# Optimization experiments

Hardware: AMD Instinct MI355X
Metric: run time of the kernel (lower is better)

The kernel has to match this reference:

```python
import math
from itertools import combinations_with_replacement
import jax, jax.numpy as jnp
import numpy as np

# ---- static config (matches init_kwargs) ----
SPECIES_LIST = [1, 6, 8]
S = len(SPECIES_LIST)
N_MAX = 8
L_MAX = 4
CUTOFF = 5.0
B, N = 4, 512

SPECIES = jnp.asarray(SPECIES_LIST, dtype=jnp.int64 if jax.config.jax_enable_x64 else jnp.int32)
PAIR_IDS = np.array(list(combinations_with_replacement(range(S), 2)), dtype=np.int32)  # (P,2)
P = PAIR_IDS.shape[0]

# orthonormalization matrix W (deterministic buffer)
def _ortho_W(n_max):
    a = np.arange(1, n_max + 1, dtype=np.float64)
    Smat = np.sqrt((5 + 2 * a[:, None]) * (5 + 2 * a[None, :])) / (5 + a[:, None] + a[None, :])
    w, v = np.linalg.eigh(Smat)
    return (v @ np.diag(w ** -0.5) @ v.T).astype(np.float32)
W_ORTHO = jnp.asarray(_ortho_W(N_MAX))

# per-l power-spectrum prefactor pi*sqrt(8/(2l+1))
PS_NORM = jnp.asarray([math.pi * math.sqrt(8.0 / (2 * l + 1)) for l in range(L_MAX + 1)], dtype=jnp.float32)
# selector: which of the 25 flattened (l,m) components belong to degree l
_l_of_m = np.concatenate([np.full(2 * l + 1, l) for l in range(L_MAX + 1)])
L_SEL = jnp.asarray((_l_of_m[None, :] == np.arange(L_MAX + 1)[:, None]).astype(np.float32))  # (L,25)
# sqrt(2) on strict-upper (n,p) entries (applied before triu gather)
_offd = np.ones((N_MAX, N_MAX), dtype=np.float32)
_offd[np.triu_indices(N_MAX, 1)] = math.sqrt(2.0)
OFFD = jnp.asarray(_offd)
IU_R, IU_C = np.triu_indices(N_MAX)
PAIR_F = jnp.asarray(np.where(PAIR_IDS[:, 0] != PAIR_IDS[:, 1], math.sqrt(2.0), 1.0).astype(np.float32))


def real_sph_harm(u):
    """Real spherical harmonics (integral normalization, homogeneous polynomial form)
    for l=0..4, evaluated on u (..., 3). Returns (..., 25). Zero vector -> l>0 vanish."""
    x, y, z = u[..., 0], u[..., 1], u[..., 2]
    x2, y2, z2 = x * x, y * y, z * z
    r2 = x2 + y2 + z2
    pi = math.pi
    s = math.sqrt
    Y = [
        jnp.full_like(x, 0.5 * s(1 / pi)),
        s(3 / (4 * pi)) * y, s(3 / (4 * pi)) * z, s(3 / (4 * pi)) * x,
        0.5 * s(15 / pi) * x * y,
        0.5 * s(15 / pi) * y * z,
        0.25 * s(5 / pi) * (3 * z2 - r2),
        0.5 * s(15 / pi) * x * z,
        0.25 * s(15 / pi) * (x2 - y2),
        0.25 * s(35 / (2 * pi)) * y * (3 * x2 - y2),
        0.5 * s(105 / pi) * x * y * z,
        0.25 * s(21 / (2 * pi)) * y * (5 * z2 - r2),
        0.25 * s(7 / pi) * z * (5 * z2 - 3 * r2),
        0.25 * s(21 / (2 * pi)) * x * (5 * z2 - r2),
        0.25 * s(105 / pi) * z * (x2 - y2),
        0.25 * s(35 / (2 * pi)) * x * (x2 - 3 * y2),
        0.75 * s(35 / pi) * x * y * (x2 - y2),
        0.75 * s(35 / (2 * pi)) * y * z * (3 * x2 - y2),
        0.75 * s(5 / pi) * x * y * (7 * z2 - r2),
        0.75 * s(5 / (2 * pi)) * y * z * (7 * z2 - 3 * r2),
        (3.0 / 16.0) * s(1 / pi) * (35 * z2 * z2 - 30 * z2 * r2 + 3 * r2 * r2),
        0.75 * s(5 / (2 * pi)) * x * z * (7 * z2 - 3 * r2),
        (3.0 / 8.0) * s(5 / pi) * (x2 - y2) * (7 * z2 - r2),
        0.75 * s(35 / (2 * pi)) * x * z * (x2 - 3 * y2),
        (3.0 / 16.0) * s(35 / pi) * (x2 * x2 - 6 * x2 * y2 + y2 * y2),
    ]
    return jnp.stack(Y, axis=-1)


def soap_forward(pos, Z):
    b, n, _ = pos.shape
    # pairwise within each frame: dvec[b,i,j] = pos[b,i] - pos[b,j]  (dst - src)
    dvec = pos[:, :, None, :] - pos[:, None, :, :]          # (B,N,N,3)
    d2 = jnp.sum(dvec * dvec, axis=-1)
    dist = jnp.where(d2 > 0, jnp.sqrt(jnp.where(d2 > 0, d2, 1.0)), 0.0)
    u = dvec / jnp.where(dist > 0, dist, 1.0)[..., None]
    Y = real_sph_harm(u) * (4.0 * math.pi)                  # (B,N,N,25)
    # radial basis (l-independent in this module); cutoff mask folds in dist>=cutoff pairs
    alpha = jnp.arange(1, N_MAX + 1, dtype=pos.dtype)
    norm_factor = jnp.sqrt(CUTOFF ** (2 * alpha + 5) / (2 * alpha + 5))
    dr = jnp.maximum(CUTOFF - dist, 0.0)[..., None]
    basis = dr ** (alpha + 2) / norm_factor * (dist < CUTOFF).astype(pos.dtype)[..., None]
    g = basis @ W_ORTHO.T                                   # (B,N,N,n_max)
    # per-species scatter-add over source atoms j -> density coefficients c
    s_oh = (Z[..., None] == SPECIES).astype(pos.dtype)      # (B,N,S)
    c = jnp.einsum('bjs,bijn,bijm->bisnm', s_oh, g, Y)      # (B,N,S,n_max,25)
    # power spectrum: sum over m within each l
    ps = jnp.einsum('bisnm,bitpm,lm->bistlnp', c, c, L_SEL) # (B,N,S,S,L,n,n)
    ps = ps[:, :, PAIR_IDS[:, 0], PAIR_IDS[:, 1]]           # (B,N,P,L,n,n)
    ps = ps * PAIR_F[:, None, None, None] * PS_NORM[:, None, None] * OFFD
    desc = ps[..., IU_R, IU_C]                              # (B,N,P,L,36)
    return desc.reshape(b, n, -1)                           # (B,N,1080)


def setup_inputs() -> dict:
    key = jax.random.key(0)
    k1, k2 = jax.random.split(key)
    pos = jax.random.uniform(k1, (B, N, 3), dtype=jnp.float32) * 22.0
    Z = SPECIES[jax.random.randint(k2, (B, N), 0, S)]
    return {'pos': pos, 'Z': Z}


def reference(pos, Z):
    return soap_forward(pos, Z)
```

## Files before the change

### kernel.cpp

```cpp
#include <hip/hip_runtime.h>
#include <cmath>

#define NMAX   8
#define NM     25
#define ROWW   40
#define NOUT   1080
#define C2SZ   1440

struct Params {
    float W[NMAX * NMAX];
    float invnorm[NMAX];
    float ycoef[NM];
    float lscale[5];
    float pairf[6];
};

__device__ __forceinline__ void neighbor_compute(const Params& prm,
                                                 float dx, float dy, float dz,
                                                 float* __restrict__ row) {
    const float d2 = dx * dx + dy * dy + dz * dz;
    const float dist = sqrtf(d2);
    const float inv  = dist > 0.f ? 1.f / dist : 0.f;
    const float x = dx * inv, y = dy * inv, z = dz * inv;
    const float x2 = x * x, y2 = y * y, z2 = z * z;
    const float r2 = x2 + y2 + z2;

    const float dr = 5.f - dist;
    float bas[NMAX];
    float drp = dr * dr * dr;
#pragma unroll
    for (int a = 0; a < NMAX; ++a) { bas[a] = drp * prm.invnorm[a]; drp *= dr; }
    float g[NMAX];
#pragma unroll
    for (int n = 0; n < NMAX; ++n) {
        float acc = 0.f;
#pragma unroll
        for (int a = 0; a < NMAX; ++a) acc += bas[a] * prm.W[n * NMAX + a];
        g[n] = acc;
    }

    float Yv[NM];
    Yv[0]  = prm.ycoef[0];
    Yv[1]  = prm.ycoef[1]  * y;
    Yv[2]  = prm.ycoef[2]  * z;
    Yv[3]  = prm.ycoef[3]  * x;
    Yv[4]  = prm.ycoef[4]  * x * y;
    Yv[5]  = prm.ycoef[5]  * y * z;
    Yv[6]  = prm.ycoef[6]  * (3.f * z2 - r2);
    Yv[7]  = prm.ycoef[7]  * x * z;
    Yv[8]  = prm.ycoef[8]  * (x2 - y2);
    Yv[9]  = prm.ycoef[9]  * y * (3.f * x2 - y2);
    Yv[10] = prm.ycoef[10] * x * y * z;
    Yv[11] = prm.ycoef[11] * y * (5.f * z2 - r2);
    Yv[12] = prm.ycoef[12] * z * (5.f * z2 - 3.f * r2);
    Yv[13] = prm.ycoef[13] * x * (5.f * z2 - r2);
    Yv[14] = prm.ycoef[14] * z * (x2 - y2);
    Yv[15] = prm.ycoef[15] * x * (x2 - 3.f * y2);
    Yv[16] = prm.ycoef[16] * x * y * (x2 - y2);
    Yv[17] = prm.ycoef[17] * y * z * (3.f * x2 - y2);
    Yv[18] = prm.ycoef[18] * x * y * (7.f * z2 - r2);
    Yv[19] = prm.ycoef[19] * y * z * (7.f * z2 - 3.f * r2);
    Yv[20] = prm.ycoef[20] * (35.f * z2 * z2 - 30.f * z2 * r2 + 3.f * r2 * r2);
    Yv[21] = prm.ycoef[21] * x * z * (7.f * z2 - 3.f * r2);
    Yv[22] = prm.ycoef[22] * (x2 - y2) * (7.f * z2 - r2);
    Yv[23] = prm.ycoef[23] * x * z * (x2 - 3.f * y2);
    Yv[24] = prm.ycoef[24] * (x2 * x2 - 6.f * x2 * y2 + y2 * y2);

    float4* q = (float4*)row;
    q[0] = make_float4(g[0], g[1], g[2], g[3]);
    q[1] = make_float4(g[4], g[5], g[6], g[7]);
    q[2] = make_float4(Yv[0], Yv[8],  Yv[16], Yv[24]);
    q[3] = make_float4(Yv[1], Yv[9],  Yv[17], 0.f);
    q[4] = make_float4(Yv[2], Yv[10], Yv[18], 0.f);
    q[5] = make_float4(Yv[3], Yv[11], Yv[19], 0.f);
    q[6] = make_float4(Yv[4], Yv[12], Yv[20], 0.f);
    q[7] = make_float4(Yv[5], Yv[13], Yv[21], 0.f);
    q[8] = make_float4(Yv[6], Yv[14], Yv[22], 0.f);
    q[9] = make_float4(Yv[7], Yv[15], Yv[23], 0.f);
}

__global__ __launch_bounds__(64)
void soap_kernel(const float* __restrict__ pos, const int* __restrict__ Z,
                 float* __restrict__ out, Params prm) {
    __shared__ __align__(16) float gys[64 * ROWW];
    __shared__ float4 dA[64];
    __shared__ float4 dB[64];
    __shared__ __align__(16) float c2[C2SZ];
    __shared__ int spl[64];

    const int lane = threadIdx.x;
    const int site = blockIdx.x;
    const int jbase = (site >> 9) << 9;

    const float xi = pos[site * 3 + 0];
    const float yi = pos[site * 3 + 1];
    const float zi = pos[site * 3 + 2];

    {
        float4* c4 = (float4*)c2;
        const float4 zz4 = make_float4(0.f, 0.f, 0.f, 0.f);
#pragma unroll
        for (int i = 0; i < 5; ++i) c4[i * 64 + lane] = zz4;
        if (lane < 40) c4[320 + lane] = zz4;
    }

    const unsigned long long ltm = (1ull << lane) - 1ull;
    int mtot = 0;
#pragma unroll
    for (int it = 0; it < 8; ++it) {
        const int ja = jbase + it * 64 + lane;
        const float dx = xi - pos[ja * 3 + 0];
        const float dy = yi - pos[ja * 3 + 1];
        const float dz = zi - pos[ja * 3 + 2];
        const float d2 = dx * dx + dy * dy + dz * dz;
        const bool pr = d2 < 25.0f;
        const unsigned long long mk = __ballot(pr);
        if (pr) {
            const int sl = mtot + __popcll(mk & ltm);
            if (sl < 64) dA[sl] = make_float4(dx, dy, dz, (float)ja);
        }
        mtot += __popcll(mk);
    }
    const int M = mtot;

    const int n_own = lane & 7;
    const int mrow  = lane >> 3;
    float a0[4] = {0.f,0.f,0.f,0.f};
    float a1[4] = {0.f,0.f,0.f,0.f};
    float a2[4] = {0.f,0.f,0.f,0.f};

    if (M <= 64) {
        float4 v = make_float4(0.f, 0.f, 0.f, 0.f);
        int sp = -1;
        if (lane < M) {
            v = dA[lane];
            const int zz = Z[(int)v.w];
            sp = (zz == 1) ? 0 : (zz == 6) ? 1 : 2;
        }
        const unsigned long long b0 = __ballot(sp == 0);
        const unsigned long long b1 = __ballot(sp == 1);
        const unsigned long long b2 = __ballot(sp == 2);
        const int R1 = __popcll(b0);
        const int R2 = R1 + __popcll(b1);
        int np = -1;
        if (sp == 0)      np = __popcll(b0 & ltm);
        else if (sp == 1) np = R1 + __popcll(b1 & ltm);
        else if (sp == 2) np = R2 + __popcll(b2 & ltm);
        if (np >= 0) dB[np] = v;

        if (lane < M) {
            const float4 u = dB[lane];
            neighbor_compute(prm, u.x, u.y, u.z, &gys[lane * ROWW]);
        }

        const float* yb = &gys[8 + 4 * mrow];
#pragma unroll 2
        for (int sl = 0; sl < R1; ++sl) {
            const float g = gys[sl * ROWW + n_own];
            const float4 y4 = *(const float4*)&yb[sl * ROWW];
            a0[0] += g * y4.x; a0[1] += g * y4.y; a0[2] += g * y4.z; a0[3] += g * y4.w;
        }
#pragma unroll 2
        for (int sl = R1; sl < R2; ++sl) {
            const float g = gys[sl * ROWW + n_own];
            const float4 y4 = *(const float4*)&yb[sl * ROWW];
            a1[0] += g * y4.x; a1[1] += g * y4.y; a1[2] += g * y4.z; a1[3] += g * y4.w;
        }
#pragma unroll 2
        for (int sl = R2; sl < M; ++sl) {
            const float g = gys[sl * ROWW + n_own];
            const float4 y4 = *(const float4*)&yb[sl * ROWW];
            a2[0] += g * y4.x; a2[1] += g * y4.y; a2[2] += g * y4.z; a2[3] += g * y4.w;
        }
    } else {
        for (int it = 0; it < 8; ++it) {
            const int ja = jbase + it * 64 + lane;
            const float dx = xi - pos[ja * 3 + 0];
            const float dy = yi - pos[ja * 3 + 1];
            const float dz = zi - pos[ja * 3 + 2];
            const float d2 = dx * dx + dy * dy + dz * dz;
            const bool pr = d2 < 25.0f;
            const unsigned long long mk = __ballot(pr);
            const int cnt = __popcll(mk);
            if (pr) {
                const int sl = __popcll(mk & ltm);
                dA[sl] = make_float4(dx, dy, dz, 0.f);
                const int zz = Z[ja];
                spl[sl] = (zz == 1) ? 0 : (zz == 6) ? 1 : 2;
            }
            if (lane < cnt) {
                const float4 u = dA[lane];
                neighbor_compute(prm, u.x, u.y, u.z, &gys[lane * ROWW]);
            }
            const float* yb = &gys[8 + 4 * mrow];
            for (int sl = 0; sl < cnt; ++sl) {
                const int ss = spl[sl];
                const float g = gys[sl * ROWW + n_own];
                const float4 y4 = *(const float4*)&yb[sl * ROWW];
                if (ss == 0) {
                    a0[0] += g * y4.x; a0[1] += g * y4.y; a0[2] += g * y4.z; a0[3] += g * y4.w;
                } else if (ss == 1) {
                    a1[0] += g * y4.x; a1[1] += g * y4.y; a1[2] += g * y4.z; a1[3] += g * y4.w;
                } else {
                    a2[0] += g * y4.x; a2[1] += g * y4.y; a2[2] += g * y4.z; a2[3] += g * y4.w;
                }
            }
        }
    }

#pragma unroll
    for (int k = 0; k < 4; ++k) {
        const int m = mrow + 8 * k;
        if (m < NM) {
            const int l  = (int)sqrtf((float)m);
            const int kk = m - l * l;
            const int idx = l * 288 + n_own * 12 + kk;
            c2[idx      ] = a0[k];
            c2[idx +  96] = a1[k];
            c2[idx + 192] = a2[k];
        }
    }

#pragma unroll
    for (int it = 0; it < 17; ++it) {
        const int o = it * 64 + lane;
        if (o < NOUT) {
            const int q   = o / 180;
            const int rem = o - q * 180;
            const int l   = rem / 36;
            const int t   = rem - l * 36;
            const int n = (int)((17.0f - sqrtf((float)(289 - 8 * t))) * 0.5f);
            const int p = t - ((n * (17 - n)) >> 1) + n;
            const int s1 = (q < 3) ? 0 : ((q < 5) ? 1 : 2);
            const int s2 = (q < 3) ? q : ((q < 5) ? (q - 2) : 2);
            const float4* ra = (const float4*)&c2[l * 288 + s1 * 96 + n * 12];
            const float4* rb = (const float4*)&c2[l * 288 + s2 * 96 + p * 12];
            const float4 A0 = ra[0], B0 = rb[0];
            const float4 A1 = ra[1], B1 = rb[1];
            const float4 A2 = ra[2], B2 = rb[2];
            float sum = A0.x * B0.x + A0.y * B0.y + A0.z * B0.z + A0.w * B0.w
                      + A1.x * B1.x + A1.y * B1.y + A1.z * B1.z + A1.w * B1.w
                      + A2.x * B2.x + A2.y * B2.y + A2.z * B2.z + A2.w * B2.w;
            float sc = prm.pairf[q] * prm.lscale[l];
            if (n != p) sc *= 1.41421356237309515f;
            out[site * NOUT + o] = sum * sc;
        }
    }
}

extern "C" void kernel_launch(void* const* d_in, const int* in_sizes, int n_in,
                              void* d_out, int out_size, void* d_ws, size_t ws_size,
                              hipStream_t stream) {
    const float* pos = (const float*)d_in[0];
    const int*   Z   = (const int*)d_in[1];
    float*       out = (float*)d_out;
    const int nsite  = in_sizes[1];

    Params prm;

    double A[8][8], V[8][8];
    for (int i = 0; i < 8; ++i)
        for (int j = 0; j < 8; ++j) {
            const double ai = i + 1.0, aj = j + 1.0;
            A[i][j] = sqrt((5.0 + 2.0 * ai) * (5.0 + 2.0 * aj)) / (5.0 + ai + aj);
            V[i][j] = (i == j) ? 1.0 : 0.0;
        }
    for (int sweep = 0; sweep < 30; ++sweep) {
        for (int p = 0; p < 8; ++p)
            for (int q = p + 1; q < 8; ++q) {
                const double apq = A[p][q];
                if (fabs(apq) < 1e-300) continue;
                const double phi = 0.5 * atan2(2.0 * apq, A[q][q] - A[p][p]);
                const double c = cos(phi), s = sin(phi);
                for (int k = 0; k < 8; ++k) {
                    const double akp = A[k][p], akq = A[k][q];
                    A[k][p] = c * akp - s * akq;
                    A[k][q] = s * akp + c * akq;
                }
                for (int k = 0; k < 8; ++k) {
                    const double apk = A[p][k], aqk = A[q][k];
                    A[p][k] = c * apk - s * aqk;
                    A[q][k] = s * apk + c * aqk;
                }
                for (int k = 0; k < 8; ++k) {
                    const double vkp = V[k][p], vkq = V[k][q];
                    V[k][p] = c * vkp - s * vkq;
                    V[k][q] = s * vkp + c * vkq;
                }
            }
    }
    for (int i = 0; i < 8; ++i)
        for (int j = 0; j < 8; ++j) {
            double acc = 0.0;
            for (int k = 0; k < 8; ++k) acc += V[i][k] * V[j][k] / sqrt(A[k][k]);
            prm.W[i * 8 + j] = (float)acc;
        }

    for (int a = 0; a < 8; ++a)
        prm.invnorm[a] = (float)(1.0 / sqrt(pow(5.0, 2.0 * a + 7.0) / (2.0 * a + 7.0)));

    const double pi = 3.14159265358979323846;
    const double fp = 4.0 * pi;
    double yc[NM];
    yc[0]  = 0.5 * sqrt(1.0 / pi);
    yc[1]  = yc[2] = yc[3] = sqrt(3.0 / (4.0 * pi));
    yc[4]  = yc[5] = yc[7] = 0.5 * sqrt(15.0 / pi);
    yc[6]  = 0.25 * sqrt(5.0 / pi);
    yc[8]  = 0.25 * sqrt(15.0 / pi);
    yc[9]  = yc[15] = 0.25 * sqrt(35.0 / (2.0 * pi));
    yc[10] = 0.5 * sqrt(105.0 / pi);
    yc[11] = yc[13] = 0.25 * sqrt(21.0 / (2.0 * pi));
    yc[12] = 0.25 * sqrt(7.0 / pi);
    yc[14] = 0.25 * sqrt(105.0 / pi);
    yc[16] = 0.75 * sqrt(35.0 / pi);
    yc[17] = yc[23] = 0.75 * sqrt(35.0 / (2.0 * pi));
    yc[18] = 0.75 * sqrt(5.0 / pi);
    yc[19] = yc[21] = 0.75 * sqrt(5.0 / (2.0 * pi));
    yc[20] = 3.0 / 16.0 * sqrt(1.0 / pi);
    yc[22] = 3.0 / 8.0 * sqrt(5.0 / pi);
    yc[24] = 3.0 / 16.0 * sqrt(35.0 / pi);
    for (int m = 0; m < NM; ++m) prm.ycoef[m] = (float)(yc[m] * fp);

    for (int l = 0; l <= 4; ++l) prm.lscale[l] = (float)(pi * sqrt(8.0 / (2.0 * l + 1.0)));
    const float rt2 = 1.41421356237309515f;
    prm.pairf[0] = 1.f; prm.pairf[1] = rt2; prm.pairf[2] = rt2;
    prm.pairf[3] = 1.f; prm.pairf[4] = rt2; prm.pairf[5] = 1.f;

    soap_kernel<<<nsite, 64, 0, stream>>>(pos, Z, out, prm);
}
```

Baseline: 16.84 us.

## Split density accumulation across per-species wavefronts in 256-thread blocks

Each block now runs four wavefronts. Three of them each filter neighbours for one species and accumulate that species' density coefficients, in a smaller chunked shared buffer. A block-wide sync follows, then all four waves compute the power-spectrum items using a compacted per-l layout that skips the zero padding. The aim is to parallelise the serial per-site accumulation and cut wasted FMAs on padded m entries. In exchange, every wave recomputes the distance filter, the fourth wave sits idle during accumulation, and the larger blocks may lower occupancy.

```diff
diff --git a/kernel.cpp b/kernel.cpp
--- a/kernel.cpp
+++ b/kernel.cpp
@@ -1,11 +1,13 @@
 #include <hip/hip_runtime.h>
 #include <cmath>
 
-#define NMAX   8
-#define NM     25
-#define ROWW   40
-#define NOUT   1080
-#define C2SZ   1440
+#define NMAX    8
+#define NM      25
+#define GSLOTS  24
+#define ROWW    44
+#define NOUT    1080
+#define CROW    36
+#define CSLICE  288
 
 struct Params {
     float W[NMAX * NMAX];
@@ -79,171 +81,133 @@
     q[9] = make_float4(Yv[7], Yv[15], Yv[23], 0.f);
 }
 
-__global__ __launch_bounds__(64)
+__global__ __launch_bounds__(256)
 void soap_kernel(const float* __restrict__ pos, const int* __restrict__ Z,
                  float* __restrict__ out, Params prm) {
-    __shared__ __align__(16) float gys[64 * ROWW];
-    __shared__ float4 dA[64];
-    __shared__ float4 dB[64];
-    __shared__ __align__(16) float c2[C2SZ];
-    __shared__ int spl[64];
-
-    const int lane = threadIdx.x;
+    __shared__ float4 dA[3][64];
+    __shared__ __align__(16) float gys[3][GSLOTS * ROWW];
+    __shared__ __align__(16) float c2[3 * CSLICE];
+
+    const int tid  = threadIdx.x;
+    const int lane = tid & 63;
+    const int w    = tid >> 6;
     const int site = blockIdx.x;
     const int jbase = (site >> 9) << 9;
+    const unsigned long long ltm = (1ull << lane) - 1ull;
 
     const float xi = pos[site * 3 + 0];
     const float yi = pos[site * 3 + 1];
     const float zi = pos[site * 3 + 2];
 
-    {
-        float4* c4 = (float4*)c2;
-        const float4 zz4 = make_float4(0.f, 0.f, 0.f, 0.f);
-#pragma unroll
-        for (int i = 0; i < 5; ++i) c4[i * 64 + lane] = zz4;
-        if (lane < 40) c4[320 + lane] = zz4;
-    }
-
-    const unsigned long long ltm = (1ull << lane) - 1ull;
-    int mtot = 0;
-#pragma unroll
-    for (int it = 0; it < 8; ++it) {
-        const int ja = jbase + it * 64 + lane;
-        const float dx = xi - pos[ja * 3 + 0];
-        const float dy = yi - pos[ja * 3 + 1];
-        const float dz = zi - pos[ja * 3 + 2];
-        const float d2 = dx * dx + dy * dy + dz * dz;
-        const bool pr = d2 < 25.0f;
-        const unsigned long long mk = __ballot(pr);
-        if (pr) {
-            const int sl = mtot + __popcll(mk & ltm);
-            if (sl < 64) dA[sl] = make_float4(dx, dy, dz, (float)ja);
-        }
-        mtot += __popcll(mk);
-    }
-    const int M = mtot;
-
-    const int n_own = lane & 7;
-    const int mrow  = lane >> 3;
-    float a0[4] = {0.f,0.f,0.f,0.f};
-    float a1[4] = {0.f,0.f,0.f,0.f};
-    float a2[4] = {0.f,0.f,0.f,0.f};
-
-    if (M <= 64) {
-        float4 v = make_float4(0.f, 0.f, 0.f, 0.f);
-        int sp = -1;
-        if (lane < M) {
-            v = dA[lane];
-            const int zz = Z[(int)v.w];
-            sp = (zz == 1) ? 0 : (zz == 6) ? 1 : 2;
-        }
-        const unsigned long long b0 = __ballot(sp == 0);
-        const unsigned long long b1 = __ballot(sp == 1);
-        const unsigned long long b2 = __ballot(sp == 2);
-        const int R1 = __popcll(b0);
-        const int R2 = R1 + __popcll(b1);
-        int np = -1;
-        if (sp == 0)      np = __popcll(b0 & ltm);
-        else if (sp == 1) np = R1 + __popcll(b1 & ltm);
-        else if (sp == 2) np = R2 + __popcll(b2 & ltm);
-        if (np >= 0) dB[np] = v;
-
-        if (lane < M) {
-            const float4 u = dB[lane];
-            neighbor_compute(prm, u.x, u.y, u.z, &gys[lane * ROWW]);
-        }
-
-        const float* yb = &gys[8 + 4 * mrow];
-#pragma unroll 2
-        for (int sl = 0; sl < R1; ++sl) {
-            const float g = gys[sl * ROWW + n_own];
-            const float4 y4 = *(const float4*)&yb[sl * ROWW];
-            a0[0] += g * y4.x; a0[1] += g * y4.y; a0[2] += g * y4.z; a0[3] += g * y4.w;
-        }
-#pragma unroll 2
-        for (int sl = R1; sl < R2; ++sl) {
-            const float g = gys[sl * ROWW + n_own];
-            const float4 y4 = *(const float4*)&yb[sl * ROWW];
-            a1[0] += g * y4.x; a1[1] += g * y4.y; a1[2] += g * y4.z; a1[3] += g * y4.w;
-        }
-#pragma unroll 2
-        for (int sl = R2; sl < M; ++sl) {
-            const float g = gys[sl * ROWW + n_own];
-            const float4 y4 = *(const float4*)&yb[sl * ROWW];
-            a2[0] += g * y4.x; a2[1] += g * y4.y; a2[2] += g * y4.z; a2[3] += g * y4.w;
-        }
-    } else {
+    if (w < 3) {
+        const int s = w;
+        float4* cz = (float4*)&c2[s * CSLICE];
+        cz[lane & 63] = make_float4(0.f, 0.f, 0.f, 0.f);
+        if (lane < 8) cz[64 + lane] = make_float4(0.f, 0.f, 0.f, 0.f);
+
+        int mtot = 0;
+#pragma unroll
         for (int it = 0; it < 8; ++it) {
             const int ja = jbase + it * 64 + lane;
             const float dx = xi - pos[ja * 3 + 0];
             const float dy = yi - pos[ja * 3 + 1];
             const float dz = zi - pos[ja * 3 + 2];
             const float d2 = dx * dx + dy * dy + dz * dz;
-            const bool pr = d2 < 25.0f;
+            const int zz = Z[ja];
+            const int sp = (zz == 1) ? 0 : (zz == 6) ? 1 : 2;
+            const bool pr = (d2 < 25.0f) && (sp == s);
             const unsigned long long mk = __ballot(pr);
-            const int cnt = __popcll(mk);
             if (pr) {
-                const int sl = __popcll(mk & ltm);
-                dA[sl] = make_float4(dx, dy, dz, 0.f);
+                const int sl = mtot + __popcll(mk & ltm);
+                if (sl < 64) dA[s][sl] = make_float4(dx, dy, dz, 0.f);
+            }
+            mtot += __popcll(mk);
+        }
+        const int Ms = mtot;
+
+        const int n_own = lane & 7;
+        const int mrow  = lane >> 3;
+        float a[4] = {0.f, 0.f, 0.f, 0.f};
+        const float* yb = &gys[s][8 + 4 * mrow];
+
+        if (Ms <= 64) {
+            for (int rb = 0; rb < Ms; rb += GSLOTS) {
+                const int cnt = min(GSLOTS, Ms - rb);
+                if (lane < cnt) {
+                    const float4 u = dA[s][rb + lane];
+                    neighbor_compute(prm, u.x, u.y, u.z, &gys[s][lane * ROWW]);
+                }
+                for (int sl = 0; sl < cnt; ++sl) {
+                    const float g  = gys[s][sl * ROWW + n_own];
+                    const float4 y4 = *(const float4*)&yb[sl * ROWW];
+                    a[0] += g * y4.x; a[1] += g * y4.y; a[2] += g * y4.z; a[3] += g * y4.w;
+                }
+            }
+        } else {
+            for (int it = 0; it < 8; ++it) {
+                const int ja = jbase + it * 64 + lane;
+                const float dx = xi - pos[ja * 3 + 0];
+                const float dy = yi - pos[ja * 3 + 1];
+                const float dz = zi - pos[ja * 3 + 2];
+                const float d2 = dx * dx + dy * dy + dz * dz;
                 const int zz = Z[ja];
-                spl[sl] = (zz == 1) ? 0 : (zz == 6) ? 1 : 2;
-            }
-            if (lane < cnt) {
-                const float4 u = dA[lane];
-                neighbor_compute(prm, u.x, u.y, u.z, &gys[lane * ROWW]);
-            }
-            const float* yb = &gys[8 + 4 * mrow];
-            for (int sl = 0; sl < cnt; ++sl) {
-                const int ss = spl[sl];
-                const float g = gys[sl * ROWW + n_own];
-                const float4 y4 = *(const float4*)&yb[sl * ROWW];
-                if (ss == 0) {
-                    a0[0] += g * y4.x; a0[1] += g * y4.y; a0[2] += g * y4.z; a0[3] += g * y4.w;
-                } else if (ss == 1) {
-                    a1[0] += g * y4.x; a1[1] += g * y4.y; a1[2] += g * y4.z; a1[3] += g * y4.w;
-                } else {
-                    a2[0] += g * y4.x; a2[1] += g * y4.y; a2[2] += g * y4.z; a2[3] += g * y4.w;
-                }
-            }
-        }
-    }
-
-#pragma unroll
-    for (int k = 0; k < 4; ++k) {
-        const int m = mrow + 8 * k;
-        if (m < NM) {
-            const int l  = (int)sqrtf((float)m);
-            const int kk = m - l * l;
-            const int idx = l * 288 + n_own * 12 + kk;
-            c2[idx      ] = a0[k];
-            c2[idx +  96] = a1[k];
-            c2[idx + 192] = a2[k];
-        }
-    }
-
-#pragma unroll
-    for (int it = 0; it < 17; ++it) {
-        const int o = it * 64 + lane;
-        if (o < NOUT) {
-            const int q   = o / 180;
-            const int rem = o - q * 180;
-            const int l   = rem / 36;
-            const int t   = rem - l * 36;
-            const int n = (int)((17.0f - sqrtf((float)(289 - 8 * t))) * 0.5f);
-            const int p = t - ((n * (17 - n)) >> 1) + n;
+                const int sp = (zz == 1) ? 0 : (zz == 6) ? 1 : 2;
+                const bool pr = (d2 < 25.0f) && (sp == s);
+                const unsigned long long mk = __ballot(pr);
+                const int cnt0 = __popcll(mk);
+                if (pr) dA[s][__popcll(mk & ltm)] = make_float4(dx, dy, dz, 0.f);
+                for (int rb = 0; rb < cnt0; rb += GSLOTS) {
+                    const int cnt = min(GSLOTS, cnt0 - rb);
+                    if (lane < cnt) {
+                        const float4 u = dA[s][rb + lane];
+                        neighbor_compute(prm, u.x, u.y, u.z, &gys[s][lane * ROWW]);
+                    }
+                    for (int sl = 0; sl < cnt; ++sl) {
+                        const float g  = gys[s][sl * ROWW + n_own];
+                        const float4 y4 = *(const float4*)&yb[sl * ROWW];
+                        a[0] += g * y4.x; a[1] += g * y4.y; a[2] += g * y4.z; a[3] += g * y4.w;
+                    }
+                }
+            }
+        }
+
+#pragma unroll
+        for (int k = 0; k < 4; ++k) {
+            const int m = mrow + 8 * k;
+            if (m < NM) {
+                const int l  = (int)sqrtf((float)m);
+                const int kk = m - l * l;
+                const int lofs = (l < 2) ? 4 * l : 8 * (l - 1);
+                c2[s * CSLICE + n_own * CROW + lofs + kk] = a[k];
+            }
+        }
+    }
+
+    __syncthreads();
+
+    if (lane < 36) {
+        const int t = lane;
+        const int n = (int)((17.0f - sqrtf((float)(289 - 8 * t))) * 0.5f);
+        const int p = t - ((n * (17 - n)) >> 1) + n;
+        const float npf = (n != p) ? 1.41421356237309515f : 1.0f;
+        const int start = (w < 2) ? 8 * w : 16 + 7 * (w - 2);
+        const int icnt  = (w < 2) ? 8 : 7;
+        for (int ii = 0; ii < icnt; ++ii) {
+            const int item = start + ii;
+            const int q = (item * 13) >> 6;
+            const int l = item - 5 * q;
             const int s1 = (q < 3) ? 0 : ((q < 5) ? 1 : 2);
             const int s2 = (q < 3) ? q : ((q < 5) ? (q - 2) : 2);
-            const float4* ra = (const float4*)&c2[l * 288 + s1 * 96 + n * 12];
-            const float4* rb = (const float4*)&c2[l * 288 + s2 * 96 + p * 12];
-            const float4 A0 = ra[0], B0 = rb[0];
-            const float4 A1 = ra[1], B1 = rb[1];
-            const float4 A2 = ra[2], B2 = rb[2];
-            float sum = A0.x * B0.x + A0.y * B0.y + A0.z * B0.z + A0.w * B0.w
-                      + A1.x * B1.x + A1.y * B1.y + A1.z * B1.z + A1.w * B1.w
-                      + A2.x * B2.x + A2.y * B2.y + A2.z * B2.z + A2.w * B2.w;
-            float sc = prm.pairf[q] * prm.lscale[l];
-            if (n != p) sc *= 1.41421356237309515f;
-            out[site * NOUT + o] = sum * sc;
+            const int lofs = (l < 2) ? 4 * l : 8 * (l - 1);
+            const int nq   = (l < 2) ? 1 : ((l < 4) ? 2 : 3);
+            const float4* ra = (const float4*)&c2[s1 * CSLICE + n * CROW + lofs];
+            const float4* rb = (const float4*)&c2[s2 * CSLICE + p * CROW + lofs];
+            float sum = 0.f;
+            for (int j = 0; j < nq; ++j) {
+                const float4 av = ra[j], bv = rb[j];
+                sum += av.x * bv.x + av.y * bv.y + av.z * bv.z + av.w * bv.w;
+            }
+            out[site * NOUT + q * 180 + l * 36 + t] = sum * prm.pairf[q] * prm.lscale[l] * npf;
         }
     }
 }
@@ -326,5 +290,5 @@
     prm.pairf[0] = 1.f; prm.pairf[1] = rt2; prm.pairf[2] = rt2;
     prm.pairf[3] = 1.f; prm.pairf[4] = rt2; prm.pairf[5] = 1.f;
 
-    soap_kernel<<<nsite, 64, 0, stream>>>(pos, Z, out, prm);
+    soap_kernel<<<nsite, 256, 0, stream>>>(pos, Z, out, prm);
 }
```

Result: slower. 21.29 us (+26.4%).

## Pad species groups to four rows, unroll accumulation, compact c2 layout

Applied to the files above, without the earlier changes.

The species index is now computed during the neighbour scan and packed into the float4, so the second gather of Z is no longer needed. Each species group is padded to a multiple of four zero-filled rows, which lets the accumulation loop process four neighbours per step without remainder handling. The c2 buffer switches to a per-species, per-n layout with variable-length l segments, so the power-spectrum dot products load only the needed float4s instead of a fixed twelve floats. It also sets a launch bound of 2 blocks and zeroes a larger slab, adding shared-memory stores and variable-trip loops in return.

```diff
diff --git a/kernel.cpp b/kernel.cpp
--- a/kernel.cpp
+++ b/kernel.cpp
@@ -1,11 +1,13 @@
 #include <hip/hip_runtime.h>
 #include <cmath>
 
-#define NMAX   8
-#define NM     25
-#define ROWW   40
-#define NOUT   1080
-#define C2SZ   1440
+#define NMAX     8
+#define NM       25
+#define ROWW     40
+#define SLABROWS 76
+#define NOUT     1080
+#define CROW     36
+#define CSLICE   288
 
 struct Params {
     float W[NMAX * NMAX];
@@ -79,32 +81,24 @@
     q[9] = make_float4(Yv[7], Yv[15], Yv[23], 0.f);
 }
 
-__global__ __launch_bounds__(64)
+__global__ __launch_bounds__(64, 2)
 void soap_kernel(const float* __restrict__ pos, const int* __restrict__ Z,
                  float* __restrict__ out, Params prm) {
-    __shared__ __align__(16) float gys[64 * ROWW];
     __shared__ float4 dA[64];
-    __shared__ float4 dB[64];
-    __shared__ __align__(16) float c2[C2SZ];
+    __shared__ float4 dB[SLABROWS];
+    __shared__ __align__(16) float slab[SLABROWS * ROWW];
+    __shared__ __align__(16) float c2[3 * CSLICE];
     __shared__ int spl[64];
 
     const int lane = threadIdx.x;
     const int site = blockIdx.x;
     const int jbase = (site >> 9) << 9;
+    const unsigned long long ltm = (1ull << lane) - 1ull;
 
     const float xi = pos[site * 3 + 0];
     const float yi = pos[site * 3 + 1];
     const float zi = pos[site * 3 + 2];
 
-    {
-        float4* c4 = (float4*)c2;
-        const float4 zz4 = make_float4(0.f, 0.f, 0.f, 0.f);
-#pragma unroll
-        for (int i = 0; i < 5; ++i) c4[i * 64 + lane] = zz4;
-        if (lane < 40) c4[320 + lane] = zz4;
-    }
-
-    const unsigned long long ltm = (1ull << lane) - 1ull;
     int mtot = 0;
 #pragma unroll
     for (int it = 0; it < 8; ++it) {
@@ -112,16 +106,34 @@
         const float dx = xi - pos[ja * 3 + 0];
         const float dy = yi - pos[ja * 3 + 1];
         const float dz = zi - pos[ja * 3 + 2];
+        const int zz = Z[ja];
         const float d2 = dx * dx + dy * dy + dz * dz;
+        const int sp = (zz == 1) ? 0 : (zz == 6) ? 1 : 2;
         const bool pr = d2 < 25.0f;
         const unsigned long long mk = __ballot(pr);
         if (pr) {
             const int sl = mtot + __popcll(mk & ltm);
-            if (sl < 64) dA[sl] = make_float4(dx, dy, dz, (float)ja);
+            if (sl < 64) dA[sl] = make_float4(dx, dy, dz, __int_as_float(sp));
         }
         mtot += __popcll(mk);
     }
     const int M = mtot;
+
+    {
+        float4* sq = (float4*)slab;
+        const float4 z4 = make_float4(0.f, 0.f, 0.f, 0.f);
+#pragma unroll
+        for (int it = 0; it < 12; ++it) {
+            const int i = it * 64 + lane;
+            if (i < SLABROWS * 10) sq[i] = z4;
+        }
+        float4* cq = (float4*)c2;
+#pragma unroll
+        for (int it = 0; it < 4; ++it) {
+            const int i = it * 64 + lane;
+            if (i < 216) cq[i] = z4;
+        }
+    }
 
     const int n_own = lane & 7;
     const int mrow  = lane >> 3;
@@ -132,46 +144,56 @@
     if (M <= 64) {
         float4 v = make_float4(0.f, 0.f, 0.f, 0.f);
         int sp = -1;
-        if (lane < M) {
-            v = dA[lane];
-            const int zz = Z[(int)v.w];
-            sp = (zz == 1) ? 0 : (zz == 6) ? 1 : 2;
-        }
-        const unsigned long long b0 = __ballot(sp == 0);
-        const unsigned long long b1 = __ballot(sp == 1);
-        const unsigned long long b2 = __ballot(sp == 2);
-        const int R1 = __popcll(b0);
-        const int R2 = R1 + __popcll(b1);
+        if (lane < M) { v = dA[lane]; sp = __float_as_int(v.w); }
+        const unsigned long long bb0 = __ballot(sp == 0);
+        const unsigned long long bb1 = __ballot(sp == 1);
+        const unsigned long long bb2 = __ballot(sp == 2);
+        const int n0 = __popcll(bb0), n1 = __popcll(bb1), n2 = __popcll(bb2);
+        const int n0p = (n0 + 3) & ~3, n1p = (n1 + 3) & ~3, n2p = (n2 + 3) & ~3;
+        const int base1 = n0p, base2 = n0p + n1p, Mp = base2 + n2p;
         int np = -1;
-        if (sp == 0)      np = __popcll(b0 & ltm);
-        else if (sp == 1) np = R1 + __popcll(b1 & ltm);
-        else if (sp == 2) np = R2 + __popcll(b2 & ltm);
+        if (sp == 0)      np = __popcll(bb0 & ltm);
+        else if (sp == 1) np = base1 + __popcll(bb1 & ltm);
+        else if (sp == 2) np = base2 + __popcll(bb2 & ltm);
         if (np >= 0) dB[np] = v;
 
-        if (lane < M) {
-            const float4 u = dB[lane];
-            neighbor_compute(prm, u.x, u.y, u.z, &gys[lane * ROWW]);
-        }
-
-        const float* yb = &gys[8 + 4 * mrow];
-#pragma unroll 2
-        for (int sl = 0; sl < R1; ++sl) {
-            const float g = gys[sl * ROWW + n_own];
-            const float4 y4 = *(const float4*)&yb[sl * ROWW];
-            a0[0] += g * y4.x; a0[1] += g * y4.y; a0[2] += g * y4.z; a0[3] += g * y4.w;
-        }
-#pragma unroll 2
-        for (int sl = R1; sl < R2; ++sl) {
-            const float g = gys[sl * ROWW + n_own];
-            const float4 y4 = *(const float4*)&yb[sl * ROWW];
-            a1[0] += g * y4.x; a1[1] += g * y4.y; a1[2] += g * y4.z; a1[3] += g * y4.w;
-        }
-#pragma unroll 2
-        for (int sl = R2; sl < M; ++sl) {
-            const float g = gys[sl * ROWW + n_own];
-            const float4 y4 = *(const float4*)&yb[sl * ROWW];
-            a2[0] += g * y4.x; a2[1] += g * y4.y; a2[2] += g * y4.z; a2[3] += g * y4.w;
-        }
+        for (int rb = 0; rb < Mp; rb += 64) {
+            const int row = rb + lane;
+            bool real;
+            if (row < base1)      real = row < n0;
+            else if (row < base2) real = (row - base1) < n1;
+            else                  real = (row - base2) < n2;
+            if (real && row < Mp) {
+                const float4 u = dB[row];
+                neighbor_compute(prm, u.x, u.y, u.z, &slab[row * ROWW]);
+            }
+        }
+
+#define BGROUP(ACC, RSTART, REND)                                              \
+        for (int r = (RSTART); r < (REND); r += 4) {                           \
+            const float* rp = &slab[r * ROWW];                                 \
+            const float g0 = rp[n_own];                                        \
+            const float g1 = rp[ROWW + n_own];                                 \
+            const float g2 = rp[2 * ROWW + n_own];                             \
+            const float g3 = rp[3 * ROWW + n_own];                             \
+            const float* yp = rp + 8 + 4 * mrow;                               \
+            const float4 y0 = *(const float4*)(yp);                            \
+            const float4 y1 = *(const float4*)(yp + ROWW);                     \
+            const float4 y2 = *(const float4*)(yp + 2 * ROWW);                 \
+            const float4 y3 = *(const float4*)(yp + 3 * ROWW);                 \
+            ACC[0] += g0 * y0.x; ACC[1] += g0 * y0.y;                          \
+            ACC[2] += g0 * y0.z; ACC[3] += g0 * y0.w;                          \
+            ACC[0] += g1 * y1.x; ACC[1] += g1 * y1.y;                          \
+            ACC[2] += g1 * y1.z; ACC[3] += g1 * y1.w;                          \
+            ACC[0] += g2 * y2.x; ACC[1] += g2 * y2.y;                          \
+            ACC[2] += g2 * y2.z; ACC[3] += g2 * y2.w;                          \
+            ACC[0] += g3 * y3.x; ACC[1] += g3 * y3.y;                          \
+            ACC[2] += g3 * y3.z; ACC[3] += g3 * y3.w;                          \
+        }
+        BGROUP(a0, 0,     n0p)
+        BGROUP(a1, base1, base1 + n1p)
+        BGROUP(a2, base2, base2 + n2p)
+#undef BGROUP
     } else {
         for (int it = 0; it < 8; ++it) {
             const int ja = jbase + it * 64 + lane;
@@ -190,12 +212,12 @@
             }
             if (lane < cnt) {
                 const float4 u = dA[lane];
-                neighbor_compute(prm, u.x, u.y, u.z, &gys[lane * ROWW]);
-            }
-            const float* yb = &gys[8 + 4 * mrow];
+                neighbor_compute(prm, u.x, u.y, u.z, &slab[lane * ROWW]);
+            }
+            const float* yb = &slab[8 + 4 * mrow];
             for (int sl = 0; sl < cnt; ++sl) {
                 const int ss = spl[sl];
-                const float g = gys[sl * ROWW + n_own];
+                const float g = slab[sl * ROWW + n_own];
                 const float4 y4 = *(const float4*)&yb[sl * ROWW];
                 if (ss == 0) {
                     a0[0] += g * y4.x; a0[1] += g * y4.y; a0[2] += g * y4.z; a0[3] += g * y4.w;
@@ -211,13 +233,14 @@
 #pragma unroll
     for (int k = 0; k < 4; ++k) {
         const int m = mrow + 8 * k;
-        if (m < NM) {
+        if (k < 3 || mrow == 0) {
             const int l  = (int)sqrtf((float)m);
             const int kk = m - l * l;
-            const int idx = l * 288 + n_own * 12 + kk;
-            c2[idx      ] = a0[k];
-            c2[idx +  96] = a1[k];
-            c2[idx + 192] = a2[k];
+            const int lofs = (l < 2) ? 4 * l : 8 * (l - 1);
+            const int idx = n_own * CROW + lofs + kk;
+            c2[idx             ] = a0[k];
+            c2[idx +     CSLICE] = a1[k];
+            c2[idx + 2 * CSLICE] = a2[k];
         }
     }
 
@@ -233,14 +256,15 @@
             const int p = t - ((n * (17 - n)) >> 1) + n;
             const int s1 = (q < 3) ? 0 : ((q < 5) ? 1 : 2);
             const int s2 = (q < 3) ? q : ((q < 5) ? (q - 2) : 2);
-            const float4* ra = (const float4*)&c2[l * 288 + s1 * 96 + n * 12];
-            const float4* rb = (const float4*)&c2[l * 288 + s2 * 96 + p * 12];
-            const float4 A0 = ra[0], B0 = rb[0];
-            const float4 A1 = ra[1], B1 = rb[1];
-            const float4 A2 = ra[2], B2 = rb[2];
-            float sum = A0.x * B0.x + A0.y * B0.y + A0.z * B0.z + A0.w * B0.w
-                      + A1.x * B1.x + A1.y * B1.y + A1.z * B1.z + A1.w * B1.w
-                      + A2.x * B2.x + A2.y * B2.y + A2.z * B2.z + A2.w * B2.w;
+            const int lofs = (l < 2) ? 4 * l : 8 * (l - 1);
+            const int nq   = (l < 2) ? 1 : ((l < 4) ? 2 : 3);
+            const float4* ra = (const float4*)&c2[s1 * CSLICE + n * CROW + lofs];
+            const float4* rb = (const float4*)&c2[s2 * CSLICE + p * CROW + lofs];
+            float sum = 0.f;
+            for (int j = 0; j < nq; ++j) {
+                const float4 av = ra[j], bv = rb[j];
+                sum += av.x * bv.x + av.y * bv.y + av.z * bv.z + av.w * bv.w;
+            }
             float sc = prm.pairf[q] * prm.lscale[l];
             if (n != p) sc *= 1.41421356237309515f;
             out[site * NOUT + o] = sum * sc;
```

Result: slower. 21.06 us (+25.1%).

## Split SOAP into density and power-spectrum kernels with neighbor-half parallelism

Applied to the files above, without the earlier changes.

Splits the fused per-site kernel into two launches. The first computes density coefficients, with each site's 512 neighbors split across two 64-thread blocks, and writes partial coefficients to workspace. The second uses 256 threads per site to sum the partials, repack them into a per-l compact layout, and compute the 1080 outputs. The compact layout skips zero-padded m entries in the dot products. This trades more parallelism and a shorter serial tail for an extra launch and a global-memory round trip. The fused kernel is kept as a fallback when workspace is too small.

```diff
diff --git a/kernel.cpp b/kernel.cpp
--- a/kernel.cpp
+++ b/kernel.cpp
@@ -1,11 +1,14 @@
 #include <hip/hip_runtime.h>
 #include <cmath>
 
-#define NMAX   8
-#define NM     25
-#define ROWW   40
-#define NOUT   1080
-#define C2SZ   1440
+#define NMAX    8
+#define NM      25
+#define ROWW    40
+#define SLABR   48
+#define NOUT    1080
+#define CROW    36
+#define CSLICE  288
+#define CDENSE  600
 
 struct Params {
     float W[NMAX * NMAX];
@@ -79,18 +82,209 @@
     q[9] = make_float4(Yv[7], Yv[15], Yv[23], 0.f);
 }
 
+template<int NCHUNK>
 __global__ __launch_bounds__(64)
-void soap_kernel(const float* __restrict__ pos, const int* __restrict__ Z,
-                 float* __restrict__ out, Params prm) {
-    __shared__ __align__(16) float gys[64 * ROWW];
+void soap_c_kernel(const float* __restrict__ pos, const int* __restrict__ Z,
+                   float* __restrict__ ws, Params prm) {
     __shared__ float4 dA[64];
     __shared__ float4 dB[64];
-    __shared__ __align__(16) float c2[C2SZ];
+    __shared__ __align__(16) float slab[SLABR * ROWW];
+    __shared__ int spl[64];
+
+    const int lane = threadIdx.x;
+    const int wid  = blockIdx.x;
+    const int PLOG = (NCHUNK == 4) ? 1 : 0;
+    const int site = wid >> PLOG;
+    const int h    = wid & ((1 << PLOG) - 1);
+    const int jbase = (site >> 9) << 9;
+    const unsigned long long ltm = (1ull << lane) - 1ull;
+
+    const float xi = pos[site * 3 + 0];
+    const float yi = pos[site * 3 + 1];
+    const float zi = pos[site * 3 + 2];
+
+    int mtot = 0;
+#pragma unroll
+    for (int it = 0; it < NCHUNK; ++it) {
+        const int ja = jbase + (h * NCHUNK + it) * 64 + lane;
+        const float dx = xi - pos[ja * 3 + 0];
+        const float dy = yi - pos[ja * 3 + 1];
+        const float dz = zi - pos[ja * 3 + 2];
+        const float d2 = dx * dx + dy * dy + dz * dz;
+        const bool pr = d2 < 25.0f;
+        const unsigned long long mk = __ballot(pr);
+        if (pr) {
+            const int sl = mtot + __popcll(mk & ltm);
+            if (sl < 64) dA[sl] = make_float4(dx, dy, dz, (float)ja);
+        }
+        mtot += __popcll(mk);
+    }
+    const int M = mtot;
+
+    const int n_own = lane & 7;
+    const int mrow  = lane >> 3;
+    float a0[4] = {0.f,0.f,0.f,0.f};
+    float a1[4] = {0.f,0.f,0.f,0.f};
+    float a2[4] = {0.f,0.f,0.f,0.f};
+
+    if (M <= 64) {
+        float4 v = make_float4(0.f, 0.f, 0.f, 0.f);
+        int sp = -1;
+        if (lane < M) {
+            v = dA[lane];
+            const int zz = Z[(int)v.w];
+            sp = (zz == 1) ? 0 : (zz == 6) ? 1 : 2;
+        }
+        const unsigned long long b0 = __ballot(sp == 0);
+        const unsigned long long b1 = __ballot(sp == 1);
+        const unsigned long long b2 = __ballot(sp == 2);
+        const int R1 = __popcll(b0);
+        const int R2 = R1 + __popcll(b1);
+        int np = -1;
+        if (sp == 0)      np = __popcll(b0 & ltm);
+        else if (sp == 1) np = R1 + __popcll(b1 & ltm);
+        else if (sp == 2) np = R2 + __popcll(b2 & ltm);
+        if (np >= 0) dB[np] = v;
+
+        const float* yb = &slab[8 + 4 * mrow];
+        for (int rb = 0; rb < M; rb += SLABR) {
+            const int k = min(SLABR, M - rb);
+            if (lane < k) {
+                const float4 u = dB[rb + lane];
+                neighbor_compute(prm, u.x, u.y, u.z, &slab[lane * ROWW]);
+            }
+#pragma unroll 2
+            for (int sl = 0; sl < k; ++sl) {
+                const int gsl = rb + sl;
+                const float g  = slab[sl * ROWW + n_own];
+                const float4 y4 = *(const float4*)&yb[sl * ROWW];
+                if (gsl < R1) {
+                    a0[0] += g * y4.x; a0[1] += g * y4.y; a0[2] += g * y4.z; a0[3] += g * y4.w;
+                } else if (gsl < R2) {
+                    a1[0] += g * y4.x; a1[1] += g * y4.y; a1[2] += g * y4.z; a1[3] += g * y4.w;
+                } else {
+                    a2[0] += g * y4.x; a2[1] += g * y4.y; a2[2] += g * y4.z; a2[3] += g * y4.w;
+                }
+            }
+        }
+    } else {
+        for (int it = 0; it < NCHUNK; ++it) {
+            const int ja = jbase + (h * NCHUNK + it) * 64 + lane;
+            const float dx = xi - pos[ja * 3 + 0];
+            const float dy = yi - pos[ja * 3 + 1];
+            const float dz = zi - pos[ja * 3 + 2];
+            const float d2 = dx * dx + dy * dy + dz * dz;
+            const bool pr = d2 < 25.0f;
+            const unsigned long long mk = __ballot(pr);
+            const int cnt = __popcll(mk);
+            if (pr) {
+                const int sl = __popcll(mk & ltm);
+                dA[sl] = make_float4(dx, dy, dz, 0.f);
+                const int zz = Z[ja];
+                spl[sl] = (zz == 1) ? 0 : (zz == 6) ? 1 : 2;
+            }
+            if (lane < cnt) {
+                const float4 u = dA[lane];
+                neighbor_compute(prm, u.x, u.y, u.z, &slab[lane * ROWW]);
+            }
+            const float* yb = &slab[8 + 4 * mrow];
+            for (int sl = 0; sl < cnt; ++sl) {
+                const int ss = spl[sl];
+                const float g = slab[sl * ROWW + n_own];
+                const float4 y4 = *(const float4*)&yb[sl * ROWW];
+                if (ss == 0) {
+                    a0[0] += g * y4.x; a0[1] += g * y4.y; a0[2] += g * y4.z; a0[3] += g * y4.w;
+                } else if (ss == 1) {
+                    a1[0] += g * y4.x; a1[1] += g * y4.y; a1[2] += g * y4.z; a1[3] += g * y4.w;
+                } else {
+                    a2[0] += g * y4.x; a2[1] += g * y4.y; a2[2] += g * y4.z; a2[3] += g * y4.w;
+                }
+            }
+        }
+    }
+
+    const int base = wid * CDENSE + n_own * NM;
+#pragma unroll
+    for (int k = 0; k < 4; ++k) {
+        const int m = mrow + 8 * k;
+        if (k < 3 || mrow == 0) {
+            ws[base + m          ] = a0[k];
+            ws[base + m + 200    ] = a1[k];
+            ws[base + m + 400    ] = a2[k];
+        }
+    }
+}
+
+template<int PARTS>
+__global__ __launch_bounds__(256)
+void soap_out_kernel(const float* __restrict__ ws, float* __restrict__ out, Params prm) {
+    __shared__ __align__(16) float c2[3 * CSLICE];
+    const int tid  = threadIdx.x;
+    const int site = blockIdx.x;
+
+    if (tid < 216) ((float4*)c2)[tid] = make_float4(0.f, 0.f, 0.f, 0.f);
+    __syncthreads();
+
+    const int base = site * CDENSE * PARTS;
+#pragma unroll
+    for (int it = 0; it < 3; ++it) {
+        const int i = it * 256 + tid;
+        if (i < CDENSE) {
+            float v = ws[base + i];
+            if (PARTS == 2) v += ws[base + CDENSE + i];
+            const int s = i / 200;
+            const int r = i - s * 200;
+            const int n = r / 25;
+            const int m = r - n * 25;
+            const int l  = (int)sqrtf((float)m);
+            const int kk = m - l * l;
+            const int lofs = (l < 2) ? 4 * l : 8 * (l - 1);
+            c2[s * CSLICE + n * CROW + lofs + kk] = v;
+        }
+    }
+    __syncthreads();
+
+#pragma unroll
+    for (int it = 0; it < 5; ++it) {
+        const int o = it * 256 + tid;
+        if (o < NOUT) {
+            const int q   = o / 180;
+            const int rem = o - q * 180;
+            const int l   = rem / 36;
+            const int t   = rem - l * 36;
+            const int n = (int)((17.0f - sqrtf((float)(289 - 8 * t))) * 0.5f);
+            const int p = t - ((n * (17 - n)) >> 1) + n;
+            const int s1 = (q < 3) ? 0 : ((q < 5) ? 1 : 2);
+            const int s2 = (q < 3) ? q : ((q < 5) ? (q - 2) : 2);
+            const int lofs = (l < 2) ? 4 * l : 8 * (l - 1);
+            const int nq   = (l < 2) ? 1 : ((l < 4) ? 2 : 3);
+            const float4* ra = (const float4*)&c2[s1 * CSLICE + n * CROW + lofs];
+            const float4* rb = (const float4*)&c2[s2 * CSLICE + p * CROW + lofs];
+            float sum = 0.f;
+            for (int j = 0; j < nq; ++j) {
+                const float4 av = ra[j], bv = rb[j];
+                sum += av.x * bv.x + av.y * bv.y + av.z * bv.z + av.w * bv.w;
+            }
+            float sc = prm.pairf[q] * prm.lscale[l];
+            if (n != p) sc *= 1.41421356237309515f;
+            out[site * NOUT + o] = sum * sc;
+        }
+    }
+}
+
+__global__ __launch_bounds__(64)
+void soap_fused(const float* __restrict__ pos, const int* __restrict__ Z,
+                float* __restrict__ out, Params prm) {
+    __shared__ float4 dA[64];
+    __shared__ float4 dB[64];
+    __shared__ __align__(16) float slab[64 * ROWW];
+    __shared__ __align__(16) float c2[3 * CSLICE];
     __shared__ int spl[64];
 
     const int lane = threadIdx.x;
     const int site = blockIdx.x;
     const int jbase = (site >> 9) << 9;
+    const unsigned long long ltm = (1ull << lane) - 1ull;
 
     const float xi = pos[site * 3 + 0];
     const float yi = pos[site * 3 + 1];
@@ -98,13 +292,11 @@
 
     {
         float4* c4 = (float4*)c2;
-        const float4 zz4 = make_float4(0.f, 0.f, 0.f, 0.f);
-#pragma unroll
-        for (int i = 0; i < 5; ++i) c4[i * 64 + lane] = zz4;
-        if (lane < 40) c4[320 + lane] = zz4;
-    }
-
-    const unsigned long long ltm = (1ull << lane) - 1ull;
+        const float4 z4 = make_float4(0.f, 0.f, 0.f, 0.f);
+#pragma unroll
+        for (int i = 0; i < 4; ++i) { const int j = i * 64 + lane; if (j < 216) c4[j] = z4; }
+    }
+
     int mtot = 0;
 #pragma unroll
     for (int it = 0; it < 8; ++it) {
@@ -122,21 +314,14 @@
         mtot += __popcll(mk);
     }
     const int M = mtot;
-
     const int n_own = lane & 7;
     const int mrow  = lane >> 3;
-    float a0[4] = {0.f,0.f,0.f,0.f};
-    float a1[4] = {0.f,0.f,0.f,0.f};
-    float a2[4] = {0.f,0.f,0.f,0.f};
+    float a0[4] = {0.f,0.f,0.f,0.f}, a1[4] = {0.f,0.f,0.f,0.f}, a2[4] = {0.f,0.f,0.f,0.f};
 
     if (M <= 64) {
         float4 v = make_float4(0.f, 0.f, 0.f, 0.f);
         int sp = -1;
-        if (lane < M) {
-            v = dA[lane];
-            const int zz = Z[(int)v.w];
-            sp = (zz == 1) ? 0 : (zz == 6) ? 1 : 2;
-        }
+        if (lane < M) { v = dA[lane]; const int zz = Z[(int)v.w]; sp = (zz==1)?0:(zz==6)?1:2; }
         const unsigned long long b0 = __ballot(sp == 0);
         const unsigned long long b1 = __ballot(sp == 1);
         const unsigned long long b2 = __ballot(sp == 2);
@@ -147,28 +332,26 @@
         else if (sp == 1) np = R1 + __popcll(b1 & ltm);
         else if (sp == 2) np = R2 + __popcll(b2 & ltm);
         if (np >= 0) dB[np] = v;
-
         if (lane < M) {
             const float4 u = dB[lane];
-            neighbor_compute(prm, u.x, u.y, u.z, &gys[lane * ROWW]);
-        }
-
-        const float* yb = &gys[8 + 4 * mrow];
+            neighbor_compute(prm, u.x, u.y, u.z, &slab[lane * ROWW]);
+        }
+        const float* yb = &slab[8 + 4 * mrow];
 #pragma unroll 2
         for (int sl = 0; sl < R1; ++sl) {
-            const float g = gys[sl * ROWW + n_own];
+            const float g = slab[sl * ROWW + n_own];
             const float4 y4 = *(const float4*)&yb[sl * ROWW];
             a0[0] += g * y4.x; a0[1] += g * y4.y; a0[2] += g * y4.z; a0[3] += g * y4.w;
         }
 #pragma unroll 2
         for (int sl = R1; sl < R2; ++sl) {
-            const float g = gys[sl * ROWW + n_own];
+            const float g = slab[sl * ROWW + n_own];
             const float4 y4 = *(const float4*)&yb[sl * ROWW];
             a1[0] += g * y4.x; a1[1] += g * y4.y; a1[2] += g * y4.z; a1[3] += g * y4.w;
         }
 #pragma unroll 2
         for (int sl = R2; sl < M; ++sl) {
-            const float g = gys[sl * ROWW + n_own];
+            const float g = slab[sl * ROWW + n_own];
             const float4 y4 = *(const float4*)&yb[sl * ROWW];
             a2[0] += g * y4.x; a2[1] += g * y4.y; a2[2] += g * y4.z; a2[3] += g * y4.w;
         }
@@ -190,20 +373,16 @@
             }
             if (lane < cnt) {
                 const float4 u = dA[lane];
-                neighbor_compute(prm, u.x, u.y, u.z, &gys[lane * ROWW]);
-            }
-            const float* yb = &gys[8 + 4 * mrow];
+                neighbor_compute(prm, u.x, u.y, u.z, &slab[lane * ROWW]);
+            }
+            const float* yb = &slab[8 + 4 * mrow];
             for (int sl = 0; sl < cnt; ++sl) {
                 const int ss = spl[sl];
-                const float g = gys[sl * ROWW + n_own];
+                const float g = slab[sl * ROWW + n_own];
                 const float4 y4 = *(const float4*)&yb[sl * ROWW];
-                if (ss == 0) {
-                    a0[0] += g * y4.x; a0[1] += g * y4.y; a0[2] += g * y4.z; a0[3] += g * y4.w;
-                } else if (ss == 1) {
-                    a1[0] += g * y4.x; a1[1] += g * y4.y; a1[2] += g * y4.z; a1[3] += g * y4.w;
-                } else {
-                    a2[0] += g * y4.x; a2[1] += g * y4.y; a2[2] += g * y4.z; a2[3] += g * y4.w;
-                }
+                if (ss == 0) { a0[0]+=g*y4.x; a0[1]+=g*y4.y; a0[2]+=g*y4.z; a0[3]+=g*y4.w; }
+                else if (ss == 1) { a1[0]+=g*y4.x; a1[1]+=g*y4.y; a1[2]+=g*y4.z; a1[3]+=g*y4.w; }
+                else { a2[0]+=g*y4.x; a2[1]+=g*y4.y; a2[2]+=g*y4.z; a2[3]+=g*y4.w; }
             }
         }
     }
@@ -211,13 +390,12 @@
 #pragma unroll
     for (int k = 0; k < 4; ++k) {
         const int m = mrow + 8 * k;
-        if (m < NM) {
+        if (k < 3 || mrow == 0) {
             const int l  = (int)sqrtf((float)m);
             const int kk = m - l * l;
-            const int idx = l * 288 + n_own * 12 + kk;
-            c2[idx      ] = a0[k];
-            c2[idx +  96] = a1[k];
-            c2[idx + 192] = a2[k];
+            const int lofs = (l < 2) ? 4 * l : 8 * (l - 1);
+            const int idx = n_own * CROW + lofs + kk;
+            c2[idx] = a0[k]; c2[idx + CSLICE] = a1[k]; c2[idx + 2 * CSLICE] = a2[k];
         }
     }
 
@@ -233,14 +411,15 @@
             const int p = t - ((n * (17 - n)) >> 1) + n;
             const int s1 = (q < 3) ? 0 : ((q < 5) ? 1 : 2);
             const int s2 = (q < 3) ? q : ((q < 5) ? (q - 2) : 2);
-            const float4* ra = (const float4*)&c2[l * 288 + s1 * 96 + n * 12];
-            const float4* rb = (const float4*)&c2[l * 288 + s2 * 96 + p * 12];
-            const float4 A0 = ra[0], B0 = rb[0];
-            const float4 A1 = ra[1], B1 = rb[1];
-            const float4 A2 = ra[2], B2 = rb[2];
-            float sum = A0.x * B0.x + A0.y * B0.y + A0.z * B0.z + A0.w * B0.w
-                      + A1.x * B1.x + A1.y * B1.y + A1.z * B1.z + A1.w * B1.w
-                      + A2.x * B2.x + A2.y * B2.y + A2.z * B2.z + A2.w * B2.w;
+            const int lofs = (l < 2) ? 4 * l : 8 * (l - 1);
+            const int nq   = (l < 2) ? 1 : ((l < 4) ? 2 : 3);
+            const float4* ra = (const float4*)&c2[s1 * CSLICE + n * CROW + lofs];
+            const float4* rb = (const float4*)&c2[s2 * CSLICE + p * CROW + lofs];
+            float sum = 0.f;
+            for (int j = 0; j < nq; ++j) {
+                const float4 av = ra[j], bv = rb[j];
+                sum += av.x * bv.x + av.y * bv.y + av.z * bv.z + av.w * bv.w;
+            }
             float sc = prm.pairf[q] * prm.lscale[l];
             if (n != p) sc *= 1.41421356237309515f;
             out[site * NOUT + o] = sum * sc;
@@ -326,5 +505,17 @@
     prm.pairf[0] = 1.f; prm.pairf[1] = rt2; prm.pairf[2] = rt2;
     prm.pairf[3] = 1.f; prm.pairf[4] = rt2; prm.pairf[5] = 1.f;
 
-    soap_kernel<<<nsite, 64, 0, stream>>>(pos, Z, out, prm);
+    const size_t need2 = (size_t)nsite * 2 * CDENSE * sizeof(float);
+    const size_t need1 = (size_t)nsite * CDENSE * sizeof(float);
+    float* ws = (float*)d_ws;
+
+    if (ws_size >= need2) {
+        soap_c_kernel<4><<<nsite * 2, 64, 0, stream>>>(pos, Z, ws, prm);
+        soap_out_kernel<2><<<nsite, 256, 0, stream>>>(ws, out, prm);
+    } else if (ws_size >= need1) {
+        soap_c_kernel<8><<<nsite, 64, 0, stream>>>(pos, Z, ws, prm);
+        soap_out_kernel<1><<<nsite, 256, 0, stream>>>(ws, out, prm);
+    } else {
+        soap_fused<<<nsite, 64, 0, stream>>>(pos, Z, out, prm);
+    }
 }
```

After: 25.77 us. +53.0%, slower.
